# Optimization experiments

Hardware: AMD Instinct MI355X
Metric: run time of the kernel (lower is better)

Reference implementation:

```python
import jax, jax.numpy as jnp
import numpy as np

V = 65536      # vocab_size_v
H = 512        # hidden_size
M = 16         # max word length (m)
N = 8192       # number of words in the ragged batch
IH = H // 4    # char embedding dim / LSTM input size
HH = H // 2    # LSTM hidden size per direction


def setup_inputs() -> dict:
    key = jax.random.key(0)
    ks = jax.random.split(key, 16)
    word_ids = jax.random.randint(ks[0], (N,), 0, V, dtype=jnp.int32)
    is_oov = jax.random.randint(ks[1], (N,), 0, 2, dtype=jnp.int32)
    char_ids = jax.random.randint(ks[2], (N, M), 0, 256, dtype=jnp.int32)
    char_lens = jax.random.randint(ks[3], (N,), 1, M + 1, dtype=jnp.int32)
    lstm_scale = 1.0 / np.sqrt(HH)
    return {
        "word_ids": word_ids,
        "is_oov": is_oov,
        "char_ids": char_ids,
        "char_lens": char_lens,
        "word_emb": jax.random.normal(ks[4], (V, H), jnp.float32) * 0.02,
        "char_emb": jax.random.normal(ks[5], (256, IH), jnp.float32) * 0.02,
        "w_ih_f": jax.random.uniform(ks[6], (4 * HH, IH), jnp.float32, -lstm_scale, lstm_scale),
        "w_hh_f": jax.random.uniform(ks[7], (4 * HH, HH), jnp.float32, -lstm_scale, lstm_scale),
        "b_ih_f": jax.random.uniform(ks[8], (4 * HH,), jnp.float32, -lstm_scale, lstm_scale),
        "b_hh_f": jax.random.uniform(ks[9], (4 * HH,), jnp.float32, -lstm_scale, lstm_scale),
        "w_ih_b": jax.random.uniform(ks[10], (4 * HH, IH), jnp.float32, -lstm_scale, lstm_scale),
        "w_hh_b": jax.random.uniform(ks[11], (4 * HH, HH), jnp.float32, -lstm_scale, lstm_scale),
        "b_ih_b": jax.random.uniform(ks[12], (4 * HH,), jnp.float32, -lstm_scale, lstm_scale),
        "b_hh_b": jax.random.uniform(ks[13], (4 * HH,), jnp.float32, -lstm_scale, lstm_scale),
        "proj_w": jax.random.normal(ks[14], (H, H), jnp.float32) * 0.02,
        "proj_b": jax.random.normal(ks[15], (H,), jnp.float32) * 0.02,
    }


def _lstm_final_hidden(x, lens, w_ih, w_hh, b_ih, b_hh):
    """Batched variable-length LSTM; returns final hidden state h_T per sequence.

    x: [N, M, IH], lens: [N]. Carry is frozen once t >= len (emulating per-word
    batch-size-1 LSTM calls on unpadded sequences). PyTorch gate order i,f,g,o.
    """
    n = x.shape[0]
    gx = jnp.einsum("nmi,gi->nmg", x, w_ih) + b_ih + b_hh        # [N, M, 4HH]
    mask = (jnp.arange(M)[None, :] < lens[:, None])[..., None]    # [N, M, 1]

    def step(carry, inp):
        h, c = carry
        g_t, m_t = inp                                            # [N,4HH], [N,1]
        g = g_t + h @ w_hh.T
        i, f, gg, o = jnp.split(g, 4, axis=-1)
        i = jax.nn.sigmoid(i)
        f = jax.nn.sigmoid(f)
        gg = jnp.tanh(gg)
        o = jax.nn.sigmoid(o)
        c_new = f * c + i * gg
        h_new = o * jnp.tanh(c_new)
        h = jnp.where(m_t, h_new, h)
        c = jnp.where(m_t, c_new, c)
        return (h, c), None

    h0 = jnp.zeros((n, HH), x.dtype)
    c0 = jnp.zeros((n, HH), x.dtype)
    (h, _), _ = jax.lax.scan(step, (h0, c0),
                             (gx.transpose(1, 0, 2), mask.transpose(1, 0, 2)))
    return h  # [N, HH]


def reference(word_ids, is_oov, char_ids, char_lens,
              word_emb, char_emb,
              w_ih_f, w_hh_f, b_ih_f, b_hh_f,
              w_ih_b, w_hh_b, b_ih_b, b_hh_b,
              proj_w, proj_b):
    # Char-level path (computed for all words, selected only where OOV).
    x = char_emb[char_ids]                                        # [N, M, IH]
    h_fwd = _lstm_final_hidden(x, char_lens, w_ih_f, w_hh_f, b_ih_f, b_hh_f)
    # Backward direction: reverse each sequence within its true length.
    rev_idx = jnp.clip(char_lens[:, None] - 1 - jnp.arange(M)[None, :], 0, M - 1)
    x_rev = jnp.take_along_axis(x, rev_idx[..., None], axis=1)    # [N, M, IH]
    h_bwd = _lstm_final_hidden(x_rev, char_lens, w_ih_b, w_hh_b, b_ih_b, b_hh_b)
    char_word_embed = jnp.concatenate([h_fwd, h_bwd], axis=-1)    # [N, H]

    vocab_embed = word_emb[word_ids]                              # [N, H]
    sel = jnp.where(is_oov[:, None] > 0, char_word_embed, vocab_embed)
    return sel @ proj_w.T + proj_b                                # [N, H]
```

## Files before the change

### kernel.cpp

```cpp
#include <hip/hip_runtime.h>
#include <math.h>

#define VOCAB   65536
#define HDIM    512
#define MLEN    16
#define NWORDS  8192
#define IHDIM   128
#define HHDIM   256

#define TMW 32
#define TP  32

#define B_WHH 0u
#define B_GX2 1048576u
#define B_PBF 5242880u
#define B_PBB 5767168u
#define B_CHE 5769216u
#define B_INT 14157824u

typedef _Float16 f16x8 __attribute__((ext_vector_type(8)));
typedef float    f32x4 __attribute__((ext_vector_type(4)));
union U4H8 { uint4 u; f16x8 h; _Float16 e[8]; };

__device__ __forceinline__ unsigned packh2(float lo, float hi) {
    union { _Float16 h[2]; unsigned u; } v;
    v.h[0] = (_Float16)lo; v.h[1] = (_Float16)hi;
    return v.u;
}

__device__ __forceinline__ float sigf(float x)  { return 1.0f / (1.0f + __expf(-x)); }
__device__ __forceinline__ float tanh_f(float x){ return 1.0f - 2.0f / (__expf(2.0f * x) + 1.0f); }

__device__ __forceinline__ void load_lds_128(const void* g, void* l) {
    __builtin_amdgcn_global_load_lds((const __attribute__((address_space(1))) unsigned*)g,
                                     (__attribute__((address_space(3))) unsigned*)l, 16, 0, 0);
}

__global__ void prep_k(const float* __restrict__ whhf, const float* __restrict__ whhb,
                       const float* __restrict__ projw, const float* __restrict__ projb,
                       char* __restrict__ wsb) {
    int i = blockIdx.x * blockDim.x + threadIdx.x;
    if (i < 65536) {
        int dir = i >> 15, r = i & 32767, kt = r >> 12, r2 = r & 4095, ntg = r2 >> 6, lane = r2 & 63;
        const float* whh = dir ? whhb : whhf;
        int n  = ntg * 16 + (lane & 15);
        int k0 = kt * 32 + (lane >> 4) * 8;
        unsigned q[4];
        #pragma unroll
        for (int jj = 0; jj < 4; ++jj)
            q[jj] = packh2(whh[n * HHDIM + k0 + 2 * jj], whh[n * HHDIM + k0 + 2 * jj + 1]);
        ((uint4*)(wsb + B_WHH))[i] = make_uint4(q[0], q[1], q[2], q[3]);
    }
    if (i < 32768) {
        int kt = i >> 11, r = i & 2047, nt = r >> 6, lane = r & 63;
        int j  = nt * 16 + (lane & 15);
        int k0 = kt * 32 + (lane >> 4) * 8;
        unsigned q[4];
        #pragma unroll
        for (int jj = 0; jj < 4; ++jj)
            q[jj] = packh2(projw[j * HDIM + k0 + 2 * jj], projw[j * HDIM + k0 + 2 * jj + 1]);
        ((uint4*)(wsb + B_PBF))[i] = make_uint4(q[0], q[1], q[2], q[3]);
    }
    if (i < 512) ((float*)(wsb + B_PBB))[i] = projb[i];
}

__global__ void gxc_k(const float* __restrict__ wihf, const float* __restrict__ wihb,
                      const float* __restrict__ bihf, const float* __restrict__ bhhf,
                      const float* __restrict__ bihb, const float* __restrict__ bhhb,
                      const float* __restrict__ chemb, char* __restrict__ wsb) {
    const int dir = blockIdx.x >> 8, cid = blockIdx.x & 255;
    __shared__ __align__(16) float emb[IHDIM];
    __shared__ float gxl[1024];
    if (threadIdx.x < IHDIM) emb[threadIdx.x] = chemb[cid * IHDIM + threadIdx.x];
    __syncthreads();
    const float* wih = dir ? wihb : wihf;
    const float* bih = dir ? bihb : bihf;
    const float* bhh = dir ? bhhb : bhhf;
    #pragma unroll
    for (int p = 0; p < 4; ++p) {
        int n = threadIdx.x + p * 256;
        float acc = bih[n] + bhh[n];
        const float4* w4 = (const float4*)(wih + n * IHDIM);
        const float4* e4 = (const float4*)emb;
        #pragma unroll 8
        for (int k4 = 0; k4 < 32; ++k4) {
            float4 w = w4[k4], e = e4[k4];
            acc = fmaf(w.x, e.x, fmaf(w.y, e.y, fmaf(w.z, e.z, fmaf(w.w, e.w, acc))));
        }
        gxl[n] = acc;
    }
    __syncthreads();
    uint4* outp = (uint4*)(wsb + B_GX2) + (size_t)(dir * 256 + cid) * 512;
    #pragma unroll
    for (int s = 0; s < 2; ++s) {
        int tid2 = threadIdx.x + s * 256;
        int wv = tid2 >> 6, col = tid2 & 15;
        U4H8 v;
        #pragma unroll
        for (int g = 0; g < 4; ++g)
            #pragma unroll
            for (int c = 0; c < 2; ++c)
                v.e[g * 2 + c] = (_Float16)gxl[g * 256 + wv * 32 + c * 16 + col];
        outp[tid2] = v.u;
    }
}

__global__ void count_k(const int* __restrict__ is_oov, const int* __restrict__ lens,
                        int* __restrict__ ip) {
    int n = blockIdx.x * blockDim.x + threadIdx.x;
    if (n < NWORDS && is_oov[n] > 0) atomicAdd(&ip[lens[n] - 1], 1);
}

__global__ void prefix_k(int* __restrict__ ip) {
    if (threadIdx.x == 0) {
        int total = 0;
        for (int b = 15; b >= 0; --b) { ip[16 + b] = total; ip[32 + b] = total; total += ip[b]; }
        ip[48] = total;
    }
}

__global__ void scatter_k(const int* __restrict__ is_oov, const int* __restrict__ lens,
                          int* __restrict__ ip) {
    int n = blockIdx.x * blockDim.x + threadIdx.x;
    if (n < NWORDS && is_oov[n] > 0) {
        int pos = atomicAdd(&ip[32 + lens[n] - 1], 1);
        ip[64 + pos] = n;
    }
}

__global__ __launch_bounds__(512, 2)
void lstm_k(const int* __restrict__ char_ids, const int* __restrict__ lens,
            const char* __restrict__ wsb, const int* __restrict__ ip) {
    const int dir = blockIdx.y;
    const int tid = threadIdx.x;
    const int total = ip[48];
    const int w0 = blockIdx.x * TMW;
    if (w0 >= total) return;
    const int wcount = min(TMW, total - w0);
    const int* sorted = ip + 64;

    __shared__ int n_s[TMW], len_s[TMW];
    __shared__ int cid_s[MLEN][TMW];
    __shared__ __align__(16) _Float16 Zh[TMW][264];
    __shared__ __align__(16) uint4 wbuf[8][2][512];

    if (tid < TMW) {
        int idx = w0 + min(tid, wcount - 1);
        n_s[tid] = sorted[idx];
        len_s[tid] = (tid < wcount) ? lens[sorted[idx]] : 0;
    }
    for (int i = tid; i < TMW * 132; i += 512) ((unsigned*)Zh)[i] = 0u;
    __syncthreads();
    {
        int m = tid >> 4, t = tid & 15;
        int L = len_s[m];
        int pos = dir ? max(L - 1 - t, 0) : t;
        cid_s[t][m] = char_ids[n_s[m] * MLEN + pos];
    }

    const int wv = tid >> 6, lane = tid & 63, col = lane & 15, quad = lane >> 4;
    int lenr[2][4];
    #pragma unroll
    for (int mt = 0; mt < 2; ++mt)
        #pragma unroll
        for (int r = 0; r < 4; ++r) lenr[mt][r] = len_s[mt * 16 + quad * 4 + r];
    const int maxlen = len_s[0];

    const uint4* wpg = (const uint4*)(wsb + B_WHH) + (size_t)dir * 32768;
    const uint4* gx2 = (const uint4*)(wsb + B_GX2) + (size_t)dir * 131072;

    float cst[2][2][4];
    #pragma unroll
    for (int c = 0; c < 2; ++c)
        #pragma unroll
        for (int mt = 0; mt < 2; ++mt)
            #pragma unroll
            for (int r = 0; r < 4; ++r) cst[c][mt][r] = 0.0f;

    auto stage = [&](int kt, int buf) {
        #pragma unroll
        for (int gc = 0; gc < 8; ++gc) {
            int ntg = (gc >> 1) * 16 + wv * 2 + (gc & 1);
            load_lds_128(wpg + (kt * 4096 + ntg * 64 + lane), &wbuf[wv][buf][gc * 64]);
        }
    };
    stage(0, 0);
    __syncthreads();

    for (int t = 0; t < maxlen; ++t) {
        U4H8 gq[2][4];
        #pragma unroll
        for (int mt = 0; mt < 2; ++mt)
            #pragma unroll
            for (int r = 0; r < 4; ++r)
                gq[mt][r].u = gx2[(size_t)cid_s[t][mt * 16 + quad * 4 + r] * 512 + tid];

        f32x4 acc[4][2][2];
        #pragma unroll
        for (int g = 0; g < 4; ++g)
            #pragma unroll
            for (int c = 0; c < 2; ++c)
                #pragma unroll
                for (int mt = 0; mt < 2; ++mt) {
                    f32x4 a;
                    #pragma unroll
                    for (int r = 0; r < 4; ++r) a[r] = (float)gq[mt][r].e[g * 2 + c];
                    acc[g][c][mt] = a;
                }

        #pragma unroll
        for (int kt = 0; kt < 8; ++kt) {
            const int buf = kt & 1;
            stage((kt + 1) & 7, buf ^ 1);
            __builtin_amdgcn_s_waitcnt(0x0F78);
            f16x8 af0 = *(const f16x8*)&Zh[col][kt * 32 + quad * 8];
            f16x8 af1 = *(const f16x8*)&Zh[16 + col][kt * 32 + quad * 8];
            #pragma unroll
            for (int g = 0; g < 4; ++g)
                #pragma unroll
                for (int c = 0; c < 2; ++c) {
                    U4H8 b; b.u = wbuf[wv][buf][(g * 2 + c) * 64 + lane];
                    acc[g][c][0] = __builtin_amdgcn_mfma_f32_16x16x32_f16(af0, b.h, acc[g][c][0], 0, 0, 0);
                    acc[g][c][1] = __builtin_amdgcn_mfma_f32_16x16x32_f16(af1, b.h, acc[g][c][1], 0, 0, 0);
                }
        }
        __syncthreads();

        #pragma unroll
        for (int mt = 0; mt < 2; ++mt)
            #pragma unroll
            for (int r = 0; r < 4; ++r) {
                if (t < lenr[mt][r]) {
                    const int m = mt * 16 + quad * 4 + r;
                    #pragma unroll
                    for (int c = 0; c < 2; ++c) {
                        float i_ = sigf(acc[0][c][mt][r]);
                        float f_ = sigf(acc[1][c][mt][r]);
                        float g_ = tanh_f(acc[2][c][mt][r]);
                        float o_ = sigf(acc[3][c][mt][r]);
                        float cn = f_ * cst[c][mt][r] + i_ * g_;
                        cst[c][mt][r] = cn;
                        Zh[m][wv * 32 + c * 16 + col] = (_Float16)(o_ * tanh_f(cn));
                    }
                }
            }
        __syncthreads();
    }

    unsigned short* cheh = (unsigned short*)(wsb + B_CHE);
    for (int i = tid; i < TMW * HHDIM; i += 512) {
        int m = i >> 8, u = i & 255;
        if (m < wcount) {
            union { _Float16 h; unsigned short s; } v; v.h = Zh[m][u];
            __builtin_nontemporal_store(v.s, cheh + (size_t)n_s[m] * HDIM + dir * HHDIM + u);
        }
    }
}

__global__ __launch_bounds__(512, 2)
void proj_k(const int* __restrict__ word_ids, const int* __restrict__ is_oov,
            const float* __restrict__ word_emb, const char* __restrict__ wsb,
            float* __restrict__ out) {
    const int tid = threadIdx.x;
    const int n0 = blockIdx.x * TP;
    __shared__ __align__(16) _Float16 Zp[TP][520];

    for (int f = tid; f < TP * 128; f += 512) {
        int w = f >> 7, s4 = f & 127;
        int n = n0 + w;
        if (is_oov[n] > 0) {
            ushort4 hv = ((const ushort4*)((const unsigned short*)(wsb + B_CHE) + (size_t)n * HDIM))[s4];
            *(ushort4*)&Zp[w][s4 * 4] = hv;
        } else {
            float4 v = ((const float4*)(word_emb + (size_t)word_ids[n] * HDIM))[s4];
            Zp[w][s4 * 4 + 0] = (_Float16)v.x;
            Zp[w][s4 * 4 + 1] = (_Float16)v.y;
            Zp[w][s4 * 4 + 2] = (_Float16)v.z;
            Zp[w][s4 * 4 + 3] = (_Float16)v.w;
        }
    }
    __syncthreads();

    const int wv = tid >> 6, lane = tid & 63, col = lane & 15, quad = lane >> 4;
    const float* pbb = (const float*)(wsb + B_PBB);
    f32x4 acc[4][2];
    #pragma unroll
    for (int c = 0; c < 4; ++c) {
        float b = pbb[wv * 64 + c * 16 + col];
        acc[c][0] = (f32x4){b, b, b, b};
        acc[c][1] = (f32x4){b, b, b, b};
    }

    const uint4* pbf = (const uint4*)(wsb + B_PBF);
    #pragma unroll
    for (int kt = 0; kt < 16; ++kt) {
        f16x8 af0 = *(const f16x8*)&Zp[col][kt * 32 + quad * 8];
        f16x8 af1 = *(const f16x8*)&Zp[16 + col][kt * 32 + quad * 8];
        #pragma unroll
        for (int c = 0; c < 4; ++c) {
            U4H8 b; b.u = pbf[(size_t)kt * 2048 + (wv * 4 + c) * 64 + lane];
            acc[c][0] = __builtin_amdgcn_mfma_f32_16x16x32_f16(af0, b.h, acc[c][0], 0, 0, 0);
            acc[c][1] = __builtin_amdgcn_mfma_f32_16x16x32_f16(af1, b.h, acc[c][1], 0, 0, 0);
        }
    }

    #pragma unroll
    for (int mt = 0; mt < 2; ++mt)
        #pragma unroll
        for (int r = 0; r < 4; ++r) {
            const size_t m = n0 + mt * 16 + quad * 4 + r;
            #pragma unroll
            for (int c = 0; c < 4; ++c)
                __builtin_nontemporal_store(acc[c][mt][r], &out[m * HDIM + wv * 64 + c * 16 + col]);
        }
}

extern "C" void kernel_launch(void* const* d_in, const int* in_sizes, int n_in,
                              void* d_out, int out_size, void* d_ws, size_t ws_size,
                              hipStream_t stream) {
    const int*   word_ids  = (const int*)d_in[0];
    const int*   is_oov    = (const int*)d_in[1];
    const int*   char_ids  = (const int*)d_in[2];
    const int*   char_lens = (const int*)d_in[3];
    const float* word_emb  = (const float*)d_in[4];
    const float* char_emb  = (const float*)d_in[5];
    const float* w_ih_f    = (const float*)d_in[6];
    const float* w_hh_f    = (const float*)d_in[7];
    const float* b_ih_f    = (const float*)d_in[8];
    const float* b_hh_f    = (const float*)d_in[9];
    const float* w_ih_b    = (const float*)d_in[10];
    const float* w_hh_b    = (const float*)d_in[11];
    const float* b_ih_b    = (const float*)d_in[12];
    const float* b_hh_b    = (const float*)d_in[13];
    const float* proj_w    = (const float*)d_in[14];
    const float* proj_b    = (const float*)d_in[15];
    float* out = (float*)d_out;
    char*  wsb = (char*)d_ws;
    int*   ip  = (int*)(wsb + B_INT);

    hipMemsetAsync(ip, 0, 256, stream);
    prep_k<<<256, 256, 0, stream>>>(w_hh_f, w_hh_b, proj_w, proj_b, wsb);
    gxc_k<<<512, 256, 0, stream>>>(w_ih_f, w_ih_b, b_ih_f, b_hh_f, b_ih_b, b_hh_b, char_emb, wsb);
    count_k<<<NWORDS / 256, 256, 0, stream>>>(is_oov, char_lens, ip);
    prefix_k<<<1, 64, 0, stream>>>(ip);
    scatter_k<<<NWORDS / 256, 256, 0, stream>>>(is_oov, char_lens, ip);
    lstm_k<<<dim3(NWORDS / TMW, 2), 512, 0, stream>>>(char_ids, char_lens, wsb, ip);
    proj_k<<<NWORDS / TP, 512, 0, stream>>>(word_ids, is_oov, word_emb, wsb, out);
}
```

Baseline: 475.2 us.

## Pin recurrent weights in registers, pipeline LDS staging, remap blocks to XCDs, widen projection tiles

Several changes at once. The LSTM kernel keeps the first three K-tiles of W_hh in registers and streams the remaining five through a double-buffered LDS pipeline with explicit waitcnt and sched_barrier control. It also replaces __syncthreads with raw s_barrier, adds the gate input after the MFMAs instead of seeding the accumulators, and maps a 1-D grid so each direction stays on a fixed set of XCDs. The gx precompute now handles four characters per block to reuse weight loads, and the projection tile grows to 64 words. Together these aim to cut global weight traffic and stalls on the recurrent critical path, at the cost of more register pressure and fragile hand-written wait counts.

```diff
diff --git a/kernel.cpp b/kernel.cpp
--- a/kernel.cpp
+++ b/kernel.cpp
@@ -9,7 +9,7 @@
 #define HHDIM   256
 
 #define TMW 32
-#define TP  32
+#define TP  64
 
 #define B_WHH 0u
 #define B_GX2 1048576u
@@ -35,6 +35,11 @@
     __builtin_amdgcn_global_load_lds((const __attribute__((address_space(1))) unsigned*)g,
                                      (__attribute__((address_space(3))) unsigned*)l, 16, 0, 0);
 }
+
+#define VMCNT16() do { __builtin_amdgcn_s_waitcnt(0x4F70); __builtin_amdgcn_sched_barrier(0); } while (0)
+#define VMCNT8()  do { __builtin_amdgcn_s_waitcnt(0x0F78); __builtin_amdgcn_sched_barrier(0); } while (0)
+#define LGKM0()   do { __builtin_amdgcn_sched_barrier(0); __builtin_amdgcn_s_waitcnt(0xC07F); \
+                       __builtin_amdgcn_sched_barrier(0); } while (0)
 
 __global__ void prep_k(const float* __restrict__ whhf, const float* __restrict__ whhb,
                        const float* __restrict__ projw, const float* __restrict__ projb,
@@ -68,40 +73,48 @@
                       const float* __restrict__ bihf, const float* __restrict__ bhhf,
                       const float* __restrict__ bihb, const float* __restrict__ bhhb,
                       const float* __restrict__ chemb, char* __restrict__ wsb) {
-    const int dir = blockIdx.x >> 8, cid = blockIdx.x & 255;
-    __shared__ __align__(16) float emb[IHDIM];
-    __shared__ float gxl[1024];
-    if (threadIdx.x < IHDIM) emb[threadIdx.x] = chemb[cid * IHDIM + threadIdx.x];
+    const int dir = blockIdx.x >> 6, grp = blockIdx.x & 63;
+    const int tid = threadIdx.x;
+    __shared__ __align__(16) float emb[4][IHDIM];
+    __shared__ float gxl[4][1024];
+    for (int i = tid; i < 4 * IHDIM; i += 256)
+        emb[i >> 7][i & 127] = chemb[(grp * 4 + (i >> 7)) * IHDIM + (i & 127)];
     __syncthreads();
     const float* wih = dir ? wihb : wihf;
     const float* bih = dir ? bihb : bihf;
     const float* bhh = dir ? bhhb : bhhf;
     #pragma unroll
     for (int p = 0; p < 4; ++p) {
-        int n = threadIdx.x + p * 256;
-        float acc = bih[n] + bhh[n];
+        int n = tid + p * 256;
+        float base = bih[n] + bhh[n];
+        float a0 = base, a1 = base, a2 = base, a3 = base;
         const float4* w4 = (const float4*)(wih + n * IHDIM);
-        const float4* e4 = (const float4*)emb;
-        #pragma unroll 8
+        #pragma unroll 4
         for (int k4 = 0; k4 < 32; ++k4) {
-            float4 w = w4[k4], e = e4[k4];
-            acc = fmaf(w.x, e.x, fmaf(w.y, e.y, fmaf(w.z, e.z, fmaf(w.w, e.w, acc))));
-        }
-        gxl[n] = acc;
+            float4 w = w4[k4];
+            float4 e0 = ((const float4*)emb[0])[k4];
+            float4 e1 = ((const float4*)emb[1])[k4];
+            float4 e2 = ((const float4*)emb[2])[k4];
+            float4 e3 = ((const float4*)emb[3])[k4];
+            a0 = fmaf(w.x, e0.x, fmaf(w.y, e0.y, fmaf(w.z, e0.z, fmaf(w.w, e0.w, a0))));
+            a1 = fmaf(w.x, e1.x, fmaf(w.y, e1.y, fmaf(w.z, e1.z, fmaf(w.w, e1.w, a1))));
+            a2 = fmaf(w.x, e2.x, fmaf(w.y, e2.y, fmaf(w.z, e2.z, fmaf(w.w, e2.w, a2))));
+            a3 = fmaf(w.x, e3.x, fmaf(w.y, e3.y, fmaf(w.z, e3.z, fmaf(w.w, e3.w, a3))));
+        }
+        gxl[0][n] = a0; gxl[1][n] = a1; gxl[2][n] = a2; gxl[3][n] = a3;
     }
     __syncthreads();
-    uint4* outp = (uint4*)(wsb + B_GX2) + (size_t)(dir * 256 + cid) * 512;
-    #pragma unroll
-    for (int s = 0; s < 2; ++s) {
-        int tid2 = threadIdx.x + s * 256;
-        int wv = tid2 >> 6, col = tid2 & 15;
+    uint4* outp = (uint4*)(wsb + B_GX2) + ((size_t)dir * 256 + grp * 4) * 512;
+    for (int i = tid; i < 4 * 512; i += 256) {
+        int cid4 = i >> 9, tid2 = i & 511;
+        int wv2 = tid2 >> 6, col2 = tid2 & 15;
         U4H8 v;
         #pragma unroll
         for (int g = 0; g < 4; ++g)
             #pragma unroll
             for (int c = 0; c < 2; ++c)
-                v.e[g * 2 + c] = (_Float16)gxl[g * 256 + wv * 32 + c * 16 + col];
-        outp[tid2] = v.u;
+                v.e[g * 2 + c] = (_Float16)gxl[cid4][g * 256 + wv2 * 32 + c * 16 + col2];
+        outp[(size_t)cid4 * 512 + tid2] = v.u;
     }
 }
 
@@ -131,10 +144,13 @@
 __global__ __launch_bounds__(512, 2)
 void lstm_k(const int* __restrict__ char_ids, const int* __restrict__ lens,
             const char* __restrict__ wsb, const int* __restrict__ ip) {
-    const int dir = blockIdx.y;
+    const int bid = blockIdx.x;
+    const int xcd = bid & 7;
+    const int dir = xcd >> 2;
+    const int bx  = (bid >> 3) * 4 + (xcd & 3);
     const int tid = threadIdx.x;
     const int total = ip[48];
-    const int w0 = blockIdx.x * TMW;
+    const int w0 = bx * TMW;
     if (w0 >= total) return;
     const int wcount = min(TMW, total - w0);
     const int* sorted = ip + 64;
@@ -169,13 +185,14 @@
     const uint4* wpg = (const uint4*)(wsb + B_WHH) + (size_t)dir * 32768;
     const uint4* gx2 = (const uint4*)(wsb + B_GX2) + (size_t)dir * 131072;
 
-    float cst[2][2][4];
-    #pragma unroll
-    for (int c = 0; c < 2; ++c)
-        #pragma unroll
-        for (int mt = 0; mt < 2; ++mt)
-            #pragma unroll
-            for (int r = 0; r < 4; ++r) cst[c][mt][r] = 0.0f;
+    uint4 breg[3][8];
+    #pragma unroll
+    for (int kt = 0; kt < 3; ++kt)
+        #pragma unroll
+        for (int gc = 0; gc < 8; ++gc) {
+            int ntg = (gc >> 1) * 16 + wv * 2 + (gc & 1);
+            breg[kt][gc] = wpg[kt * 4096 + ntg * 64 + lane];
+        }
 
     auto stage = [&](int kt, int buf) {
         #pragma unroll
@@ -184,8 +201,22 @@
             load_lds_128(wpg + (kt * 4096 + ntg * 64 + lane), &wbuf[wv][buf][gc * 64]);
         }
     };
-    stage(0, 0);
-    __syncthreads();
+
+    float cst[2][2][4];
+    #pragma unroll
+    for (int c = 0; c < 2; ++c)
+        #pragma unroll
+        for (int mt = 0; mt < 2; ++mt)
+            #pragma unroll
+            for (int r = 0; r < 4; ++r) cst[c][mt][r] = 0.0f;
+
+    int pa = 0, pb = 1;
+    stage(3, pa);
+    stage(4, pb);
+    __builtin_amdgcn_sched_barrier(0);
+    __builtin_amdgcn_s_waitcnt(0xC07F);
+    __builtin_amdgcn_s_barrier();
+    __builtin_amdgcn_sched_barrier(0);
 
     for (int t = 0; t < maxlen; ++t) {
         U4H8 gq[2][4];
@@ -194,6 +225,7 @@
             #pragma unroll
             for (int r = 0; r < 4; ++r)
                 gq[mt][r].u = gx2[(size_t)cid_s[t][mt * 16 + quad * 4 + r] * 512 + tid];
+        __builtin_amdgcn_sched_barrier(0);
 
         f32x4 acc[4][2][2];
         #pragma unroll
@@ -201,18 +233,10 @@
             #pragma unroll
             for (int c = 0; c < 2; ++c)
                 #pragma unroll
-                for (int mt = 0; mt < 2; ++mt) {
-                    f32x4 a;
-                    #pragma unroll
-                    for (int r = 0; r < 4; ++r) a[r] = (float)gq[mt][r].e[g * 2 + c];
-                    acc[g][c][mt] = a;
-                }
-
-        #pragma unroll
-        for (int kt = 0; kt < 8; ++kt) {
-            const int buf = kt & 1;
-            stage((kt + 1) & 7, buf ^ 1);
-            __builtin_amdgcn_s_waitcnt(0x0F78);
+                for (int mt = 0; mt < 2; ++mt)
+                    acc[g][c][mt] = (f32x4){0.0f, 0.0f, 0.0f, 0.0f};
+
+        auto mfma_lds = [&](int kt, int buf) {
             f16x8 af0 = *(const f16x8*)&Zh[col][kt * 32 + quad * 8];
             f16x8 af1 = *(const f16x8*)&Zh[16 + col][kt * 32 + quad * 8];
             #pragma unroll
@@ -223,8 +247,32 @@
                     acc[g][c][0] = __builtin_amdgcn_mfma_f32_16x16x32_f16(af0, b.h, acc[g][c][0], 0, 0, 0);
                     acc[g][c][1] = __builtin_amdgcn_mfma_f32_16x16x32_f16(af1, b.h, acc[g][c][1], 0, 0, 0);
                 }
-        }
-        __syncthreads();
+        };
+        auto mfma_reg = [&](const uint4 (&bs)[8], int kt) {
+            f16x8 af0 = *(const f16x8*)&Zh[col][kt * 32 + quad * 8];
+            f16x8 af1 = *(const f16x8*)&Zh[16 + col][kt * 32 + quad * 8];
+            #pragma unroll
+            for (int g = 0; g < 4; ++g)
+                #pragma unroll
+                for (int c = 0; c < 2; ++c) {
+                    U4H8 b; b.u = bs[g * 2 + c];
+                    acc[g][c][0] = __builtin_amdgcn_mfma_f32_16x16x32_f16(af0, b.h, acc[g][c][0], 0, 0, 0);
+                    acc[g][c][1] = __builtin_amdgcn_mfma_f32_16x16x32_f16(af1, b.h, acc[g][c][1], 0, 0, 0);
+                }
+        };
+
+        VMCNT16(); mfma_lds(3, pa); LGKM0(); stage(5, pa);
+        VMCNT16(); mfma_lds(4, pb); LGKM0(); stage(6, pb);
+        mfma_reg(breg[0], 0);
+        VMCNT8();  mfma_lds(5, pa); LGKM0(); stage(7, pa);
+        mfma_reg(breg[1], 1);
+        VMCNT8();  mfma_lds(6, pb); LGKM0(); stage(3, pb);
+        mfma_reg(breg[2], 2);
+        VMCNT8();  mfma_lds(7, pa); LGKM0(); stage(4, pa);
+
+        __builtin_amdgcn_sched_barrier(0);
+        __builtin_amdgcn_s_barrier();
+        __builtin_amdgcn_sched_barrier(0);
 
         #pragma unroll
         for (int mt = 0; mt < 2; ++mt)
@@ -234,17 +282,22 @@
                     const int m = mt * 16 + quad * 4 + r;
                     #pragma unroll
                     for (int c = 0; c < 2; ++c) {
-                        float i_ = sigf(acc[0][c][mt][r]);
-                        float f_ = sigf(acc[1][c][mt][r]);
-                        float g_ = tanh_f(acc[2][c][mt][r]);
-                        float o_ = sigf(acc[3][c][mt][r]);
+                        float i_ = sigf(acc[0][c][mt][r] + (float)gq[mt][r].e[0 + c]);
+                        float f_ = sigf(acc[1][c][mt][r] + (float)gq[mt][r].e[2 + c]);
+                        float g_ = tanh_f(acc[2][c][mt][r] + (float)gq[mt][r].e[4 + c]);
+                        float o_ = sigf(acc[3][c][mt][r] + (float)gq[mt][r].e[6 + c]);
                         float cn = f_ * cst[c][mt][r] + i_ * g_;
                         cst[c][mt][r] = cn;
                         Zh[m][wv * 32 + c * 16 + col] = (_Float16)(o_ * tanh_f(cn));
                     }
                 }
             }
-        __syncthreads();
+
+        LGKM0();
+        __builtin_amdgcn_s_barrier();
+        __builtin_amdgcn_sched_barrier(0);
+
+        int tsw = pa; pa = pb; pb = tsw;
     }
 
     unsigned short* cheh = (unsigned short*)(wsb + B_CHE);
@@ -283,29 +336,32 @@
 
     const int wv = tid >> 6, lane = tid & 63, col = lane & 15, quad = lane >> 4;
     const float* pbb = (const float*)(wsb + B_PBB);
-    f32x4 acc[4][2];
+    f32x4 acc[4][4];
     #pragma unroll
     for (int c = 0; c < 4; ++c) {
         float b = pbb[wv * 64 + c * 16 + col];
-        acc[c][0] = (f32x4){b, b, b, b};
-        acc[c][1] = (f32x4){b, b, b, b};
+        #pragma unroll
+        for (int mt = 0; mt < 4; ++mt) acc[c][mt] = (f32x4){b, b, b, b};
     }
 
     const uint4* pbf = (const uint4*)(wsb + B_PBF);
     #pragma unroll
     for (int kt = 0; kt < 16; ++kt) {
-        f16x8 af0 = *(const f16x8*)&Zp[col][kt * 32 + quad * 8];
-        f16x8 af1 = *(const f16x8*)&Zp[16 + col][kt * 32 + quad * 8];
+        f16x8 af[4];
+        #pragma unroll
+        for (int mt = 0; mt < 4; ++mt)
+            af[mt] = *(const f16x8*)&Zp[mt * 16 + col][kt * 32 + quad * 8];
         #pragma unroll
         for (int c = 0; c < 4; ++c) {
             U4H8 b; b.u = pbf[(size_t)kt * 2048 + (wv * 4 + c) * 64 + lane];
-            acc[c][0] = __builtin_amdgcn_mfma_f32_16x16x32_f16(af0, b.h, acc[c][0], 0, 0, 0);
-            acc[c][1] = __builtin_amdgcn_mfma_f32_16x16x32_f16(af1, b.h, acc[c][1], 0, 0, 0);
-        }
-    }
-
-    #pragma unroll
-    for (int mt = 0; mt < 2; ++mt)
+            #pragma unroll
+            for (int mt = 0; mt < 4; ++mt)
+                acc[c][mt] = __builtin_amdgcn_mfma_f32_16x16x32_f16(af[mt], b.h, acc[c][mt], 0, 0, 0);
+        }
+    }
+
+    #pragma unroll
+    for (int mt = 0; mt < 4; ++mt)
         #pragma unroll
         for (int r = 0; r < 4; ++r) {
             const size_t m = n0 + mt * 16 + quad * 4 + r;
@@ -340,10 +396,10 @@
 
     hipMemsetAsync(ip, 0, 256, stream);
     prep_k<<<256, 256, 0, stream>>>(w_hh_f, w_hh_b, proj_w, proj_b, wsb);
-    gxc_k<<<512, 256, 0, stream>>>(w_ih_f, w_ih_b, b_ih_f, b_hh_f, b_ih_b, b_hh_b, char_emb, wsb);
+    gxc_k<<<128, 256, 0, stream>>>(w_ih_f, w_ih_b, b_ih_f, b_hh_f, b_ih_b, b_hh_b, char_emb, wsb);
     count_k<<<NWORDS / 256, 256, 0, stream>>>(is_oov, char_lens, ip);
     prefix_k<<<1, 64, 0, stream>>>(ip);
     scatter_k<<<NWORDS / 256, 256, 0, stream>>>(is_oov, char_lens, ip);
-    lstm_k<<<dim3(NWORDS / TMW, 2), 512, 0, stream>>>(char_ids, char_lens, wsb, ip);
+    lstm_k<<<512, 512, 0, stream>>>(char_ids, char_lens, wsb, ip);
     proj_k<<<NWORDS / TP, 512, 0, stream>>>(word_ids, is_oov, word_emb, wsb, out);
 }
```

Measured after the change: 598.2 us. 25.9% more time.
